# Optimization experiments

Hardware: AMD Instinct MI355X
Metric: run time of the kernel (lower is better)

The kernel has to match this reference:

```python
import jax, jax.numpy as jnp
import numpy as np

V, E, H, B, S, L = 32000, 512, 1024, 128, 256, 2


def setup_inputs() -> dict:
    key = jax.random.key(0)
    ks = jax.random.split(key, 20)
    sc = 0.02
    n = lambda k, shape: jax.random.normal(k, shape, dtype=jnp.float32) * sc
    return {
        "input_ids": jax.random.randint(ks[0], (B,), 0, V),
        "h0": jax.random.normal(ks[1], (L, B, H), dtype=jnp.float32),
        "c0": jax.random.normal(ks[2], (L, B, H), dtype=jnp.float32),
        "enc_out": jax.random.normal(ks[3], (S, B, H), dtype=jnp.float32),
        "emb": n(ks[4], (V, E)),
        "w_ih0": n(ks[5], (4 * H, E)),
        "w_hh0": n(ks[6], (4 * H, H)),
        "b_ih0": n(ks[7], (4 * H,)),
        "b_hh0": n(ks[8], (4 * H,)),
        "w_ih1": n(ks[9], (4 * H, H)),
        "w_hh1": n(ks[10], (4 * H, H)),
        "b_ih1": n(ks[11], (4 * H,)),
        "b_hh1": n(ks[12], (4 * H,)),
        "attn_w": n(ks[13], (H, H)),
        "attn_b": n(ks[14], (H,)),
        "concat_w": n(ks[15], (H, 2 * H)),
        "concat_b": n(ks[16], (H,)),
        "out_w": n(ks[17], (V, H)),
        "out_b": n(ks[18], (V,)),
    }


def _lstm_step(x, h, c, w_ih, w_hh, b_ih, b_hh):
    # PyTorch gate order: i, f, g, o
    g = x @ w_ih.T + b_ih + h @ w_hh.T + b_hh  # [B, 4H]
    i, f, gg, o = jnp.split(g, 4, axis=-1)
    c_new = jax.nn.sigmoid(f) * c + jax.nn.sigmoid(i) * jnp.tanh(gg)
    h_new = jax.nn.sigmoid(o) * jnp.tanh(c_new)
    return h_new, c_new


def reference(input_ids, h0, c0, enc_out, emb, w_ih0, w_hh0, b_ih0, b_hh0,
              w_ih1, w_hh1, b_ih1, b_hh1, attn_w, attn_b, concat_w, concat_b,
              out_w, out_b):
    x = emb[input_ids]  # [B, E] (dropout is identity in eval)
    h_0, c_0 = _lstm_step(x, h0[0], c0[0], w_ih0, w_hh0, b_ih0, b_hh0)
    h_1, c_1 = _lstm_step(h_0, h0[1], c0[1], w_ih1, w_hh1, b_ih1, b_hh1)
    rnn_out = h_1  # [B, H] == rnn_output.squeeze(0)
    # Luong general attention: scores[b,s] = <W enc[s,b], rnn_out[b]>
    e_proj = enc_out @ attn_w.T + attn_b          # [S, B, H]
    scores = jnp.einsum('sbh,bh->bs', e_proj, rnn_out)  # [B, S]
    attn = jax.nn.softmax(scores, axis=-1)
    context = jnp.einsum('bs,sbh->bh', attn, enc_out)   # [B, H]
    concat_out = jnp.tanh(
        jnp.concatenate([rnn_out, context], axis=-1) @ concat_w.T + concat_b)
    logits = concat_out @ out_w.T + out_b         # [B, V]
    h_new = jnp.stack([h_0, h_1])
    c_new = jnp.stack([c_0, c_1])
    return logits, h_new, c_new
```

## Files before the change

kernel.cpp:

```cpp
#include <hip/hip_runtime.h>
#include <hip/hip_bf16.h>
#include <cstddef>
#include <cstdint>

constexpr int Bv = 128;
constexpr int Sv = 256;
constexpr int Hv = 1024;
constexpr int Ev = 512;
constexpr int Vv = 32000;

typedef __attribute__((ext_vector_type(4))) float f32x4;
typedef __attribute__((ext_vector_type(8))) short short8;

__device__ __forceinline__ uint2 cvt4(float4 v) {
  union { __hip_bfloat162 b; unsigned u; } lo, hi;
  lo.b = __float22bfloat162_rn(float2{v.x, v.y});
  hi.b = __float22bfloat162_rn(float2{v.z, v.w});
  uint2 r;
  r.x = lo.u;
  r.y = hi.u;
  return r;
}
__device__ __forceinline__ unsigned short cvt1(float x) {
  union { __hip_bfloat16 b; unsigned short u; } c;
  c.b = __float2bfloat16(x);
  return c.u;
}

template <int BM, int BN, int BK, int SPLIT, int WTR, int GATHER, int MINW>
__global__ __launch_bounds__(256, MINW) void gemm_mfma(
    const int* __restrict__ ids,
    const float* __restrict__ A1, int lda1, int K1,
    const float* __restrict__ A2, int lda2, int K2,
    const float* __restrict__ W1, int ldw1,
    const float* __restrict__ W2, int ldw2,
    const float* __restrict__ bias1, const float* __restrict__ bias2,
    float* __restrict__ C, int ldc, int N) {
  constexpr int LP = BK + 8;
  constexpr int KQ = BK / 4;
  constexpr int KSUB = BK / 32;
  constexpr int WAVES_N = (BN >= 64) ? 2 : 1;
  constexpr int WAVES_M = 4 / WAVES_N;
  constexpr int WM = BM / WAVES_M;
  constexpr int FM = WM / 16;
  constexpr int FN = BN / (16 * WAVES_N);
  constexpr int WN = FN * 16;
  constexpr int ACH = (BM * BK) / (4 * 256);
  constexpr int WCH = (BN * BK) / (4 * 256);
  constexpr int WVN = WTR ? (BK * 8 / 256) : WCH;

  __shared__ unsigned short Al[BM * LP];
  __shared__ unsigned short Wl[BN * LP];

  const int tid = threadIdx.x;
  const int wid = tid >> 6, lane = tid & 63;
  const int nBlock = blockIdx.x * BN;
  const int mBlock = blockIdx.y * BM;
  const int z = blockIdx.z;
  int wm, wn;
  if (WAVES_N == 2) { wm = (wid >> 1) * WM; wn = (wid & 1) * WN; }
  else              { wm = wid * WM;        wn = 0; }

  float4 av[ACH], wv[WVN];

  auto load_tile = [&](int kg) {
    const bool seg1 = kg < K1;
    const float* Wseg = seg1 ? W1 : W2;
    const int ldw = seg1 ? ldw1 : ldw2;
    const int kloc = seg1 ? kg : kg - K1;
#pragma unroll
    for (int i = 0; i < ACH; i++) {
      int c = tid + i * 256;
      int m = c / KQ, kq = (c % KQ) * 4;
      const float* arow;
      if (seg1) {
        if (GATHER) arow = A1 + (size_t)ids[mBlock + m] * lda1;
        else        arow = A1 + (size_t)(mBlock + m) * lda1;
      } else {
        arow = A2 + (size_t)(mBlock + m) * lda2;
      }
      av[i] = *(const float4*)(arow + kloc + kq);
    }
    if (WTR) {
#pragma unroll
      for (int i = 0; i < WVN; i++) {
        int c = tid + i * 256;
        int row = c >> 3, colq = c & 7;
        wv[i] = *(const float4*)(Wseg + (size_t)(kloc + row) * ldw + nBlock + colq * 4);
      }
    } else {
#pragma unroll
      for (int i = 0; i < WCH; i++) {
        int c = tid + i * 256;
        int n = c / KQ, kq = (c % KQ) * 4;
        wv[i] = *(const float4*)(Wseg + (size_t)(nBlock + n) * ldw + kloc + kq);
      }
    }
  };

  const int KT = K1 + K2;
  const int KS = KT / SPLIT;
  const int kbeg = z * KS;
  const int NS = KS / BK;
  load_tile(kbeg);
  f32x4 acc[FM][FN] = {};

  for (int step = 0; step < NS; ++step) {
    __syncthreads();
#pragma unroll
    for (int i = 0; i < ACH; i++) {
      int c = tid + i * 256;
      int m = c / KQ, kq = (c % KQ) * 4;
      *(uint2*)&Al[m * LP + kq] = cvt4(av[i]);
    }
    if (WTR) {
#pragma unroll
      for (int i = 0; i < WVN; i++) {
        int c = tid + i * 256;
        int row = c >> 3, colq = c & 7;
        Wl[(colq * 4 + 0) * LP + row] = cvt1(wv[i].x);
        Wl[(colq * 4 + 1) * LP + row] = cvt1(wv[i].y);
        Wl[(colq * 4 + 2) * LP + row] = cvt1(wv[i].z);
        Wl[(colq * 4 + 3) * LP + row] = cvt1(wv[i].w);
      }
    } else {
#pragma unroll
      for (int i = 0; i < WCH; i++) {
        int c = tid + i * 256;
        int n = c / KQ, kq = (c % KQ) * 4;
        *(uint2*)&Wl[n * LP + kq] = cvt4(wv[i]);
      }
    }
    __syncthreads();

    if (step + 1 < NS) load_tile(kbeg + (step + 1) * BK);

    const int klane = (lane >> 4) << 3;
    const int r = lane & 15;
    short8 af[KSUB][FM], wf[KSUB][FN];
#pragma unroll
    for (int ks = 0; ks < KSUB; ks++) {
#pragma unroll
      for (int f = 0; f < FM; f++)
        af[ks][f] = *(const short8*)&Al[(wm + f * 16 + r) * LP + ks * 32 + klane];
#pragma unroll
      for (int f = 0; f < FN; f++)
        wf[ks][f] = *(const short8*)&Wl[(wn + f * 16 + r) * LP + ks * 32 + klane];
    }
#pragma unroll
    for (int ks = 0; ks < KSUB; ks++)
#pragma unroll
      for (int fm = 0; fm < FM; fm++)
#pragma unroll
        for (int fn = 0; fn < FN; fn++)
          acc[fm][fn] = __builtin_amdgcn_mfma_f32_16x16x32_bf16(
              af[ks][fm], wf[ks][fn], acc[fm][fn], 0, 0, 0);
  }

  float* Cp = C + (size_t)z * gridDim.y * BM * ldc;
  const int col = lane & 15, rb = (lane >> 4) << 2;
#pragma unroll
  for (int fn = 0; fn < FN; fn++) {
    int n = nBlock + wn + fn * 16 + col;
    float bsum = 0.f;
    if (z == 0) {
      if (bias1) bsum += bias1[n];
      if (bias2) bsum += bias2[n];
    }
#pragma unroll
    for (int fm = 0; fm < FM; fm++) {
#pragma unroll
      for (int j = 0; j < 4; j++) {
        int m = mBlock + wm + fm * 16 + rb + j;
        Cp[(size_t)m * ldc + n] = acc[fm][fn][j] + bsum;
      }
    }
  }
}

template <int P>
__global__ void lstm_pw(const float* __restrict__ Gp,
                        const float* __restrict__ c_prev,
                        float* __restrict__ h_out,
                        float* __restrict__ c_out) {
  int i4 = blockIdx.x * 256 + threadIdx.x;
  int b = i4 >> 8, j4 = i4 & 255;
  float4 gi{}, gf{}, gg{}, go{};
#pragma unroll
  for (int p = 0; p < P; p++) {
    const float4* g = (const float4*)(Gp + (size_t)p * Bv * 4 * Hv + (size_t)b * 4096);
    float4 a = g[j4], bb = g[256 + j4], c = g[512 + j4], d = g[768 + j4];
    gi.x += a.x; gi.y += a.y; gi.z += a.z; gi.w += a.w;
    gf.x += bb.x; gf.y += bb.y; gf.z += bb.z; gf.w += bb.w;
    gg.x += c.x; gg.y += c.y; gg.z += c.z; gg.w += c.w;
    go.x += d.x; go.y += d.y; go.z += d.z; go.w += d.w;
  }
  float4 c4 = ((const float4*)c_prev)[i4];
  float4 h4, cn4;
  float* gip = &gi.x; float* gfp = &gf.x; float* ggp = &gg.x; float* gop = &go.x;
  float* cp = &c4.x; float* hp = &h4.x; float* cnp = &cn4.x;
#pragma unroll
  for (int u = 0; u < 4; u++) {
    float si = 1.f / (1.f + expf(-gip[u]));
    float sf = 1.f / (1.f + expf(-gfp[u]));
    float so = 1.f / (1.f + expf(-gop[u]));
    float cn = sf * cp[u] + si * tanhf(ggp[u]);
    hp[u] = so * tanhf(cn);
    cnp[u] = cn;
  }
  ((float4*)h_out)[i4] = h4;
  ((float4*)c_out)[i4] = cn4;
}

__global__ void scores_k(const float* __restrict__ enc,
                         const float* __restrict__ qp,
                         float* __restrict__ sc) {
  int blk = blockIdx.x;
  int b = blk >> 6, s4 = blk & 63;
  int t = threadIdx.x;
  __shared__ float qs[1024];
  {
    const float4* q0 = (const float4*)(qp + (size_t)b * Hv);
    const float4* q1 = (const float4*)(qp + 1 * Bv * Hv + (size_t)b * Hv);
    const float4* q2 = (const float4*)(qp + 2 * Bv * Hv + (size_t)b * Hv);
    const float4* q3 = (const float4*)(qp + 3 * Bv * Hv + (size_t)b * Hv);
    float4 a = q0[t], bq = q1[t], c = q2[t], d = q3[t];
    float4 s;
    s.x = a.x + bq.x + c.x + d.x; s.y = a.y + bq.y + c.y + d.y;
    s.z = a.z + bq.z + c.z + d.z; s.w = a.w + bq.w + c.w + d.w;
    ((float4*)qs)[t] = s;
  }
  __syncthreads();
  int wid = t >> 6, lane = t & 63;
  int s = s4 * 4 + wid;
  const float4* e4 = (const float4*)(enc + ((size_t)s * Bv + b) * Hv);
  const float4* q4 = (const float4*)qs;
  float sum = 0.f;
#pragma unroll
  for (int i = 0; i < 4; i++) {
    int idx = lane + i * 64;
    float4 e = e4[idx], qq = q4[idx];
    sum += e.x * qq.x + e.y * qq.y + e.z * qq.z + e.w * qq.w;
  }
#pragma unroll
  for (int o = 32; o; o >>= 1) sum += __shfl_xor(sum, o);
  if (lane == 0) sc[(size_t)b * Sv + s] = sum;
}

__global__ void context_k(const float* __restrict__ sc_in,
                          const float* __restrict__ enc,
                          float* __restrict__ ctx) {
  int blk = blockIdx.x;
  int b = blk >> 2, hc = (blk & 3) * 256;
  int t = threadIdx.x, lane = t & 63;
  __shared__ float a[256];
  __shared__ float redm[4], reds[4];
  float v = sc_in[(size_t)b * Sv + t];
  float m = v;
#pragma unroll
  for (int o = 32; o; o >>= 1) m = fmaxf(m, __shfl_xor(m, o));
  if (lane == 0) redm[t >> 6] = m;
  __syncthreads();
  m = fmaxf(fmaxf(redm[0], redm[1]), fmaxf(redm[2], redm[3]));
  float e = expf(v - m);
  float ssum = e;
#pragma unroll
  for (int o = 32; o; o >>= 1) ssum += __shfl_xor(ssum, o);
  if (lane == 0) reds[t >> 6] = ssum;
  __syncthreads();
  ssum = (reds[0] + reds[1]) + (reds[2] + reds[3]);
  a[t] = e / ssum;
  __syncthreads();

  float acc = 0.f;
  const float* ebase = enc + (size_t)b * Hv + hc + t;
#pragma unroll 8
  for (int s = 0; s < Sv; s++)
    acc += a[s] * ebase[(size_t)s * Bv * Hv];
  ctx[(size_t)b * Hv + hc + t] = acc;
}

__global__ void finish_cat(const float* __restrict__ catp,
                           float* __restrict__ cat) {
  int i4 = blockIdx.x * 256 + threadIdx.x;
  constexpr int ST = Bv * Hv / 4;
  const float4* p = (const float4*)catp;
  float4 a = p[i4], b = p[ST + i4], c = p[2 * ST + i4], d = p[3 * ST + i4];
  float4 r;
  r.x = tanhf(a.x + b.x + c.x + d.x);
  r.y = tanhf(a.y + b.y + c.y + d.y);
  r.z = tanhf(a.z + b.z + c.z + d.z);
  r.w = tanhf(a.w + b.w + c.w + d.w);
  ((float4*)cat)[i4] = r;
}

extern "C" void kernel_launch(void* const* d_in, const int* in_sizes, int n_in,
                              void* d_out, int out_size, void* d_ws,
                              size_t ws_size, hipStream_t stream) {
  const int*   ids      = (const int*)d_in[0];
  const float* h0       = (const float*)d_in[1];
  const float* c0       = (const float*)d_in[2];
  const float* enc      = (const float*)d_in[3];
  const float* emb      = (const float*)d_in[4];
  const float* w_ih0    = (const float*)d_in[5];
  const float* w_hh0    = (const float*)d_in[6];
  const float* b_ih0    = (const float*)d_in[7];
  const float* b_hh0    = (const float*)d_in[8];
  const float* w_ih1    = (const float*)d_in[9];
  const float* w_hh1    = (const float*)d_in[10];
  const float* b_ih1    = (const float*)d_in[11];
  const float* b_hh1    = (const float*)d_in[12];
  const float* attn_w   = (const float*)d_in[13];
  const float* attn_b   = (const float*)d_in[14];
  const float* concat_w = (const float*)d_in[15];
  const float* concat_b = (const float*)d_in[16];
  const float* out_w    = (const float*)d_in[17];
  const float* out_b    = (const float*)d_in[18];
  (void)attn_b;

  float* logits = (float*)d_out;
  float* hout   = logits + (size_t)Bv * Vv;
  float* cout   = hout + 2 * Bv * Hv;

  float* ws   = (float*)d_ws;
  float* G0p  = ws;
  float* G1p  = G0p + 3 * 524288;
  float* qp   = G1p + 4 * (size_t)524288;
  float* catp = qp + 4 * 131072;
  float* cat  = catp + 4 * 131072;
  float* ctx  = cat + 131072;
  float* sc   = ctx + 131072;

  const float* h_b = hout + Bv * Hv;

  gemm_mfma<64, 32, 64, 3, 0, 1, 4><<<dim3(128, 2, 3), 256, 0, stream>>>(
      ids, emb, Ev, Ev, h0, Hv, Hv, w_ih0, Ev, w_hh0, Hv, b_ih0, b_hh0,
      G0p, 4 * Hv, 4 * Hv);
  lstm_pw<3><<<128, 256, 0, stream>>>(G0p, c0, hout, cout);
  gemm_mfma<64, 32, 64, 4, 0, 0, 4><<<dim3(128, 2, 4), 256, 0, stream>>>(
      nullptr, hout, Hv, Hv, h0 + Bv * Hv, Hv, Hv, w_ih1, Hv, w_hh1, Hv,
      b_ih1, b_hh1, G1p, 4 * Hv, 4 * Hv);
  lstm_pw<4><<<128, 256, 0, stream>>>(G1p, c0 + Bv * Hv, hout + Bv * Hv,
                                      cout + Bv * Hv);
  gemm_mfma<64, 32, 64, 4, 1, 0, 4><<<dim3(32, 2, 4), 256, 0, stream>>>(
      nullptr, h_b, Hv, Hv, nullptr, 0, 0, attn_w, Hv,
      nullptr, 0, nullptr, nullptr, qp, Hv, Hv);
  scores_k<<<8192, 256, 0, stream>>>(enc, qp, sc);
  context_k<<<512, 256, 0, stream>>>(sc, enc, ctx);
  gemm_mfma<64, 32, 64, 4, 0, 0, 4><<<dim3(32, 2, 4), 256, 0, stream>>>(
      nullptr, h_b, Hv, Hv, ctx, Hv, Hv, concat_w, 2 * Hv,
      concat_w + Hv, 2 * Hv, concat_b, nullptr, catp, Hv, Hv);
  finish_cat<<<128, 256, 0, stream>>>(catp, cat);
  gemm_mfma<128, 128, 64, 1, 0, 0, 1><<<dim3(250, 1, 1), 256, 0, stream>>>(
      nullptr, cat, Hv, Hv, nullptr, 0, 0, out_w, Hv, nullptr, 0,
      out_b, nullptr, logits, Vv, Vv);
}
```

Before: 154.8 us.

## Fuse LSTM pointwise and concat tanh into split-K GEMMs via last-block counters

Removes the separate lstm_pw and finish_cat kernels. Each split-K GEMM block increments an atomic counter per output tile, and the last block to arrive reduces the partial sums and applies the LSTM gate math or the tanh epilogue. This cuts kernel launches and the extra passes over the partial buffers. In exchange it adds a counter-zeroing launch, thread fences and atomics, and serial tail work done by a single block per tile.

After: 405.5 us. +161.9%, slower.

```diff
diff --git a/kernel.cpp b/kernel.cpp
--- a/kernel.cpp
+++ b/kernel.cpp
@@ -27,7 +27,12 @@
   return c.u;
 }
 
-template <int BM, int BN, int BK, int SPLIT, int WTR, int GATHER, int MINW>
+__device__ __forceinline__ float sigm(float x) {
+  return 1.f / (1.f + expf(-x));
+}
+
+template <int BM, int BN, int BK, int SPLIT, int WTR, int GATHER, int EPI,
+          int MINW>
 __global__ __launch_bounds__(256, MINW) void gemm_mfma(
     const int* __restrict__ ids,
     const float* __restrict__ A1, int lda1, int K1,
@@ -35,7 +40,9 @@
     const float* __restrict__ W1, int ldw1,
     const float* __restrict__ W2, int ldw2,
     const float* __restrict__ bias1, const float* __restrict__ bias2,
-    float* __restrict__ C, int ldc, int N) {
+    float* __restrict__ C, int ldc, int N,
+    unsigned* ctr, const float* __restrict__ xc,
+    float* __restrict__ xh, float* __restrict__ xo) {
   constexpr int LP = BK + 8;
   constexpr int KQ = BK / 4;
   constexpr int KSUB = BK / 32;
@@ -176,40 +183,76 @@
       }
     }
   }
-}
-
-template <int P>
-__global__ void lstm_pw(const float* __restrict__ Gp,
-                        const float* __restrict__ c_prev,
-                        float* __restrict__ h_out,
-                        float* __restrict__ c_out) {
-  int i4 = blockIdx.x * 256 + threadIdx.x;
-  int b = i4 >> 8, j4 = i4 & 255;
-  float4 gi{}, gf{}, gg{}, go{};
-#pragma unroll
-  for (int p = 0; p < P; p++) {
-    const float4* g = (const float4*)(Gp + (size_t)p * Bv * 4 * Hv + (size_t)b * 4096);
-    float4 a = g[j4], bb = g[256 + j4], c = g[512 + j4], d = g[768 + j4];
-    gi.x += a.x; gi.y += a.y; gi.z += a.z; gi.w += a.w;
-    gf.x += bb.x; gf.y += bb.y; gf.z += bb.z; gf.w += bb.w;
-    gg.x += c.x; gg.y += c.y; gg.z += c.z; gg.w += c.w;
-    go.x += d.x; go.y += d.y; go.z += d.z; go.w += d.w;
-  }
-  float4 c4 = ((const float4*)c_prev)[i4];
-  float4 h4, cn4;
-  float* gip = &gi.x; float* gfp = &gf.x; float* ggp = &gg.x; float* gop = &go.x;
-  float* cp = &c4.x; float* hp = &h4.x; float* cnp = &cn4.x;
-#pragma unroll
-  for (int u = 0; u < 4; u++) {
-    float si = 1.f / (1.f + expf(-gip[u]));
-    float sf = 1.f / (1.f + expf(-gfp[u]));
-    float so = 1.f / (1.f + expf(-gop[u]));
-    float cn = sf * cp[u] + si * tanhf(ggp[u]);
-    hp[u] = so * tanhf(cn);
-    cnp[u] = cn;
-  }
-  ((float4*)h_out)[i4] = h4;
-  ((float4*)c_out)[i4] = cn4;
+
+  if (EPI == 0) return;
+
+  __syncthreads();
+  __threadfence();
+  __shared__ unsigned oldv;
+  if (tid == 0) {
+    int cidx;
+    if (EPI == 1) cidx = (blockIdx.x & 31) + 32 * blockIdx.y;
+    else          cidx = blockIdx.x + 32 * blockIdx.y;
+    oldv = __hip_atomic_fetch_add(&ctr[cidx], 1u, __ATOMIC_ACQ_REL,
+                                  __HIP_MEMORY_SCOPE_AGENT);
+  }
+  __syncthreads();
+  const unsigned TOT = (EPI == 1) ? 4u * SPLIT : (unsigned)SPLIT;
+  if (oldv != TOT - 1) return;
+
+  if (EPI == 1) {
+    const int j0 = (blockIdx.x & 31) * 32;
+#pragma unroll
+    for (int sl = 0; sl < 2; sl++) {
+      int slot = tid + sl * 256;
+      int m = mBlock + (slot >> 3), j = j0 + (slot & 7) * 4;
+      float4 gs[4] = {};
+      for (int zz = 0; zz < SPLIT; zz++) {
+        const float* gp = C + (size_t)zz * gridDim.y * BM * ldc + (size_t)m * ldc;
+#pragma unroll
+        for (int g = 0; g < 4; g++) {
+          float4 v = *(const float4*)(gp + g * 1024 + j);
+          gs[g].x += v.x; gs[g].y += v.y; gs[g].z += v.z; gs[g].w += v.w;
+        }
+      }
+      float4 c4 = *(const float4*)(xc + (size_t)m * 1024 + j);
+      float4 h4, cn4;
+      const float* gi = &gs[0].x; const float* gf = &gs[1].x;
+      const float* gg = &gs[2].x; const float* go = &gs[3].x;
+      float* cp = &c4.x; float* hp = &h4.x; float* cnp = &cn4.x;
+#pragma unroll
+      for (int u = 0; u < 4; u++) {
+        float cn = sigm(gf[u]) * cp[u] + sigm(gi[u]) * tanhf(gg[u]);
+        hp[u] = sigm(go[u]) * tanhf(cn);
+        cnp[u] = cn;
+      }
+      *(float4*)(xh + (size_t)m * 1024 + j) = h4;
+      *(float4*)(xo + (size_t)m * 1024 + j) = cn4;
+    }
+  } else {
+    const int n0 = blockIdx.x * 32;
+#pragma unroll
+    for (int sl = 0; sl < 2; sl++) {
+      int slot = tid + sl * 256;
+      int m = mBlock + (slot >> 3), j = n0 + (slot & 7) * 4;
+      const size_t st = (size_t)gridDim.y * BM * ldc;
+      const float* base = C + (size_t)m * ldc + j;
+      float4 p0 = *(const float4*)(base);
+      float4 p1 = *(const float4*)(base + st);
+      float4 p2 = *(const float4*)(base + 2 * st);
+      float4 p3 = *(const float4*)(base + 3 * st);
+      float4 r;
+      r.x = tanhf((p0.x + p1.x) + (p2.x + p3.x));
+      r.y = tanhf((p0.y + p1.y) + (p2.y + p3.y));
+      r.z = tanhf((p0.z + p1.z) + (p2.z + p3.z));
+      r.w = tanhf((p0.w + p1.w) + (p2.w + p3.w));
+      *(float4*)(xh + (size_t)m * 1024 + j) = r;
+    }
+  }
+}
+
+__global__ void zero_ctr(unsigned* c) {
+  if (threadIdx.x < 192) c[threadIdx.x] = 0;
 }
 
 __global__ void scores_k(const float* __restrict__ enc,
@@ -278,20 +321,6 @@
   for (int s = 0; s < Sv; s++)
     acc += a[s] * ebase[(size_t)s * Bv * Hv];
   ctx[(size_t)b * Hv + hc + t] = acc;
-}
-
-__global__ void finish_cat(const float* __restrict__ catp,
-                           float* __restrict__ cat) {
-  int i4 = blockIdx.x * 256 + threadIdx.x;
-  constexpr int ST = Bv * Hv / 4;
-  const float4* p = (const float4*)catp;
-  float4 a = p[i4], b = p[ST + i4], c = p[2 * ST + i4], d = p[3 * ST + i4];
-  float4 r;
-  r.x = tanhf(a.x + b.x + c.x + d.x);
-  r.y = tanhf(a.y + b.y + c.y + d.y);
-  r.z = tanhf(a.z + b.z + c.z + d.z);
-  r.w = tanhf(a.w + b.w + c.w + d.w);
-  ((float4*)cat)[i4] = r;
 }
 
 extern "C" void kernel_launch(void* const* d_in, const int* in_sizes, int n_in,
@@ -330,28 +359,30 @@
   float* cat  = catp + 4 * 131072;
   float* ctx  = cat + 131072;
   float* sc   = ctx + 131072;
+  unsigned* ctr = (unsigned*)(sc + 32768);
 
   const float* h_b = hout + Bv * Hv;
 
-  gemm_mfma<64, 32, 64, 3, 0, 1, 4><<<dim3(128, 2, 3), 256, 0, stream>>>(
+  zero_ctr<<<1, 256, 0, stream>>>(ctr);
+  gemm_mfma<64, 32, 64, 3, 0, 1, 1, 4><<<dim3(128, 2, 3), 256, 0, stream>>>(
       ids, emb, Ev, Ev, h0, Hv, Hv, w_ih0, Ev, w_hh0, Hv, b_ih0, b_hh0,
-      G0p, 4 * Hv, 4 * Hv);
-  lstm_pw<3><<<128, 256, 0, stream>>>(G0p, c0, hout, cout);
-  gemm_mfma<64, 32, 64, 4, 0, 0, 4><<<dim3(128, 2, 4), 256, 0, stream>>>(
+      G0p, 4 * Hv, 4 * Hv, ctr, c0, hout, cout);
+  gemm_mfma<64, 32, 64, 4, 0, 0, 1, 4><<<dim3(128, 2, 4), 256, 0, stream>>>(
       nullptr, hout, Hv, Hv, h0 + Bv * Hv, Hv, Hv, w_ih1, Hv, w_hh1, Hv,
-      b_ih1, b_hh1, G1p, 4 * Hv, 4 * Hv);
-  lstm_pw<4><<<128, 256, 0, stream>>>(G1p, c0 + Bv * Hv, hout + Bv * Hv,
-                                      cout + Bv * Hv);
-  gemm_mfma<64, 32, 64, 4, 1, 0, 4><<<dim3(32, 2, 4), 256, 0, stream>>>(
+      b_ih1, b_hh1, G1p, 4 * Hv, 4 * Hv, ctr + 64, c0 + Bv * Hv,
+      hout + Bv * Hv, cout + Bv * Hv);
+  gemm_mfma<64, 32, 64, 4, 1, 0, 0, 4><<<dim3(32, 2, 4), 256, 0, stream>>>(
       nullptr, h_b, Hv, Hv, nullptr, 0, 0, attn_w, Hv,
-      nullptr, 0, nullptr, nullptr, qp, Hv, Hv);
+      nullptr, 0, nullptr, nullptr, qp, Hv, Hv,
+      nullptr, nullptr, nullptr, nullptr);
   scores_k<<<8192, 256, 0, stream>>>(enc, qp, sc);
   context_k<<<512, 256, 0, stream>>>(sc, enc, ctx);
-  gemm_mfma<64, 32, 64, 4, 0, 0, 4><<<dim3(32, 2, 4), 256, 0, stream>>>(
+  gemm_mfma<64, 32, 64, 4, 0, 0, 2, 4><<<dim3(32, 2, 4), 256, 0, stream>>>(
       nullptr, h_b, Hv, Hv, ctx, Hv, Hv, concat_w, 2 * Hv,
-      concat_w + Hv, 2 * Hv, concat_b, nullptr, catp, Hv, Hv);
-  finish_cat<<<128, 256, 0, stream>>>(catp, cat);
-  gemm_mfma<128, 128, 64, 1, 0, 0, 1><<<dim3(250, 1, 1), 256, 0, stream>>>(
+      concat_w + Hv, 2 * Hv, concat_b, nullptr, catp, Hv, Hv,
+      ctr + 128, nullptr, cat, nullptr);
+  gemm_mfma<128, 128, 64, 1, 0, 0, 0, 1><<<dim3(250, 1, 1), 256, 0, stream>>>(
       nullptr, cat, Hv, Hv, nullptr, 0, 0, out_w, Hv, nullptr, 0,
-      out_b, nullptr, logits, Vv, Vv);
-}
+      out_b, nullptr, logits, Vv, Vv,
+      nullptr, nullptr, nullptr, nullptr);
+}
```

## Fuse attention scores, softmax and context into split-S partial kernel with merge

Applied to the files above, without the earlier changes.

Replaces separate scores and context kernels with a per-(batch, S-chunk) kernel that computes scores, a local softmax and a weighted partial context. A small finish kernel then merges the four chunks with rescaling by max and denominator. The encoder chunk is re-read right after being scored, so the second pass is meant to hit cache instead of HBM, and the context loop now uses float4 loads. It reuses the G0 workspace for partials, and the grid is only 512 blocks with serial per-wave score loops.

Result: slower. 159.3 us (+2.9%).

```diff
diff --git a/kernel.cpp b/kernel.cpp
--- a/kernel.cpp
+++ b/kernel.cpp
@@ -212,13 +212,14 @@
   ((float4*)c_out)[i4] = cn4;
 }
 
-__global__ void scores_k(const float* __restrict__ enc,
-                         const float* __restrict__ qp,
-                         float* __restrict__ sc) {
-  int blk = blockIdx.x;
-  int b = blk >> 6, s4 = blk & 63;
-  int t = threadIdx.x;
+__global__ __launch_bounds__(256) void attn_part(
+    const float* __restrict__ enc, const float* __restrict__ qp,
+    float* __restrict__ numb, float2* __restrict__ mden) {
+  const int b = blockIdx.x, ch = blockIdx.y;
+  const int t = threadIdx.x, lane = t & 63, wid = t >> 6;
+  const int sbase = ch * 64;
   __shared__ float qs[1024];
+  __shared__ float es[64];
   {
     const float4* q0 = (const float4*)(qp + (size_t)b * Hv);
     const float4* q1 = (const float4*)(qp + 1 * Bv * Hv + (size_t)b * Hv);
@@ -231,53 +232,70 @@
     ((float4*)qs)[t] = s;
   }
   __syncthreads();
-  int wid = t >> 6, lane = t & 63;
-  int s = s4 * 4 + wid;
-  const float4* e4 = (const float4*)(enc + ((size_t)s * Bv + b) * Hv);
+
   const float4* q4 = (const float4*)qs;
-  float sum = 0.f;
-#pragma unroll
-  for (int i = 0; i < 4; i++) {
-    int idx = lane + i * 64;
-    float4 e = e4[idx], qq = q4[idx];
-    sum += e.x * qq.x + e.y * qq.y + e.z * qq.z + e.w * qq.w;
-  }
-#pragma unroll
-  for (int o = 32; o; o >>= 1) sum += __shfl_xor(sum, o);
-  if (lane == 0) sc[(size_t)b * Sv + s] = sum;
-}
-
-__global__ void context_k(const float* __restrict__ sc_in,
-                          const float* __restrict__ enc,
-                          float* __restrict__ ctx) {
-  int blk = blockIdx.x;
-  int b = blk >> 2, hc = (blk & 3) * 256;
-  int t = threadIdx.x, lane = t & 63;
-  __shared__ float a[256];
-  __shared__ float redm[4], reds[4];
-  float v = sc_in[(size_t)b * Sv + t];
-  float m = v;
-#pragma unroll
-  for (int o = 32; o; o >>= 1) m = fmaxf(m, __shfl_xor(m, o));
-  if (lane == 0) redm[t >> 6] = m;
+  for (int i = 0; i < 16; i++) {
+    int s = sbase + wid * 16 + i;
+    const float4* e4 = (const float4*)(enc + ((size_t)s * Bv + b) * Hv);
+    float sum = 0.f;
+#pragma unroll
+    for (int j = 0; j < 4; j++) {
+      int idx = lane + j * 64;
+      float4 e = e4[idx], qq = q4[idx];
+      sum += e.x * qq.x + e.y * qq.y + e.z * qq.z + e.w * qq.w;
+    }
+#pragma unroll
+    for (int o = 32; o; o >>= 1) sum += __shfl_xor(sum, o);
+    if (lane == 0) es[wid * 16 + i] = sum;
+  }
   __syncthreads();
-  m = fmaxf(fmaxf(redm[0], redm[1]), fmaxf(redm[2], redm[3]));
-  float e = expf(v - m);
-  float ssum = e;
-#pragma unroll
-  for (int o = 32; o; o >>= 1) ssum += __shfl_xor(ssum, o);
-  if (lane == 0) reds[t >> 6] = ssum;
+
+  if (wid == 0) {
+    float v = es[lane];
+    float m = v;
+#pragma unroll
+    for (int o = 32; o; o >>= 1) m = fmaxf(m, __shfl_xor(m, o));
+    float e = expf(v - m);
+    float den = e;
+#pragma unroll
+    for (int o = 32; o; o >>= 1) den += __shfl_xor(den, o);
+    es[lane] = e;
+    if (lane == 0) mden[b * 4 + ch] = make_float2(m, den);
+  }
   __syncthreads();
-  ssum = (reds[0] + reds[1]) + (reds[2] + reds[3]);
-  a[t] = e / ssum;
-  __syncthreads();
-
-  float acc = 0.f;
-  const float* ebase = enc + (size_t)b * Hv + hc + t;
-#pragma unroll 8
-  for (int s = 0; s < Sv; s++)
-    acc += a[s] * ebase[(size_t)s * Bv * Hv];
-  ctx[(size_t)b * Hv + hc + t] = acc;
+
+  float4 acc = make_float4(0.f, 0.f, 0.f, 0.f);
+  const float* ebase = enc + ((size_t)sbase * Bv + b) * Hv + t * 4;
+#pragma unroll 4
+  for (int s = 0; s < 64; s++) {
+    float4 e = *(const float4*)(ebase + (size_t)s * Bv * Hv);
+    float w = es[s];
+    acc.x += w * e.x; acc.y += w * e.y; acc.z += w * e.z; acc.w += w * e.w;
+  }
+  *(float4*)(numb + ((size_t)ch * Bv + b) * Hv + t * 4) = acc;
+}
+
+__global__ __launch_bounds__(256) void attn_fin(
+    const float* __restrict__ numb, const float2* __restrict__ mden,
+    float* __restrict__ ctx) {
+  const int b = blockIdx.x, t = threadIdx.x;
+  float2 md0 = mden[b * 4 + 0], md1 = mden[b * 4 + 1];
+  float2 md2 = mden[b * 4 + 2], md3 = mden[b * 4 + 3];
+  float M = fmaxf(fmaxf(md0.x, md1.x), fmaxf(md2.x, md3.x));
+  float s0 = expf(md0.x - M), s1 = expf(md1.x - M);
+  float s2 = expf(md2.x - M), s3 = expf(md3.x - M);
+  float inv = 1.f / (s0 * md0.y + s1 * md1.y + s2 * md2.y + s3 * md3.y);
+  const float4* n0 = (const float4*)(numb + (size_t)b * Hv);
+  const float4* n1 = (const float4*)(numb + 1 * (size_t)Bv * Hv + (size_t)b * Hv);
+  const float4* n2 = (const float4*)(numb + 2 * (size_t)Bv * Hv + (size_t)b * Hv);
+  const float4* n3 = (const float4*)(numb + 3 * (size_t)Bv * Hv + (size_t)b * Hv);
+  float4 a = n0[t], bb = n1[t], c = n2[t], d = n3[t];
+  float4 r;
+  r.x = (s0 * a.x + s1 * bb.x + s2 * c.x + s3 * d.x) * inv;
+  r.y = (s0 * a.y + s1 * bb.y + s2 * c.y + s3 * d.y) * inv;
+  r.z = (s0 * a.z + s1 * bb.z + s2 * c.z + s3 * d.z) * inv;
+  r.w = (s0 * a.w + s1 * bb.w + s2 * c.w + s3 * d.w) * inv;
+  ((float4*)(ctx + (size_t)b * Hv))[t] = r;
 }
 
 __global__ void finish_cat(const float* __restrict__ catp,
@@ -329,7 +347,8 @@
   float* catp = qp + 4 * 131072;
   float* cat  = catp + 4 * 131072;
   float* ctx  = cat + 131072;
-  float* sc   = ctx + 131072;
+  float* numb = G0p;
+  float2* mden = (float2*)(G0p + 524288);
 
   const float* h_b = hout + Bv * Hv;
 
@@ -345,8 +364,8 @@
   gemm_mfma<64, 32, 64, 4, 1, 0, 4><<<dim3(32, 2, 4), 256, 0, stream>>>(
       nullptr, h_b, Hv, Hv, nullptr, 0, 0, attn_w, Hv,
       nullptr, 0, nullptr, nullptr, qp, Hv, Hv);
-  scores_k<<<8192, 256, 0, stream>>>(enc, qp, sc);
-  context_k<<<512, 256, 0, stream>>>(sc, enc, ctx);
+  attn_part<<<dim3(128, 4), 256, 0, stream>>>(enc, qp, numb, mden);
+  attn_fin<<<128, 256, 0, stream>>>(numb, mden, ctx);
   gemm_mfma<64, 32, 64, 4, 0, 0, 4><<<dim3(32, 2, 4), 256, 0, stream>>>(
       nullptr, h_b, Hv, Hv, ctx, Hv, Hv, concat_w, 2 * Hv,
       concat_w + Hv, 2 * Hv, concat_b, nullptr, catp, Hv, Hv);
```
